# Kernel tuning notes

Measured on AMD Instinct MI355X. Metric: run time of the kernel, lower is better.

The kernel has to match this reference:

```python
import jax, jax.numpy as jnp
import numpy as np

N, E, G = 50000, 800000, 256
H, C = 8, 16
F0 = 64
FH = H * C  # 128
L = 6
EPS = 1e-5
SEL = [0, 1, 2, 3, 4, 5, 5, 5]  # <10 layers -> pad with last


def setup_inputs() -> dict:
    key = jax.random.key(0)
    ks = jax.random.split(key, 32)

    def w(k, shape, fan_in):
        return jax.random.normal(k, shape, jnp.float32) / np.float32(np.sqrt(fan_in))

    inp = {
        'x': jax.random.normal(ks[0], (N, F0), jnp.float32),
        'edge_index': jax.random.randint(ks[1], (2, E), 0, N),
        'batch_vec': jnp.sort(jax.random.randint(ks[2], (N,), 0, G)),
        # layer 0 (in=F0)
        'Wq0': w(ks[3], (F0, FH), F0), 'bq0': 0.01 * jax.random.normal(ks[4], (FH,), jnp.float32),
        'Wk0': w(ks[5], (F0, FH), F0), 'bk0': 0.01 * jax.random.normal(ks[6], (FH,), jnp.float32),
        'Wv0': w(ks[7], (F0, FH), F0), 'bv0': 0.01 * jax.random.normal(ks[8], (FH,), jnp.float32),
        'Ws0': w(ks[9], (F0, FH), F0), 'bs0': 0.01 * jax.random.normal(ks[10], (FH,), jnp.float32),
        # layers 1..L-1 (in=FH), stacked
        'Wq': w(ks[11], (L - 1, FH, FH), FH), 'bq': 0.01 * jax.random.normal(ks[12], (L - 1, FH), jnp.float32),
        'Wk': w(ks[13], (L - 1, FH, FH), FH), 'bk': 0.01 * jax.random.normal(ks[14], (L - 1, FH), jnp.float32),
        'Wv': w(ks[15], (L - 1, FH, FH), FH), 'bv': 0.01 * jax.random.normal(ks[16], (L - 1, FH), jnp.float32),
        'Ws': w(ks[17], (L - 1, FH, FH), FH), 'bs': 0.01 * jax.random.normal(ks[18], (L - 1, FH), jnp.float32),
        # BatchNorm affine params per layer
        'gamma': jnp.ones((L, FH), jnp.float32),
        'beta': jnp.zeros((L, FH), jnp.float32),
    }
    return inp


def _transformer_conv(x, src, dst, Wq, bq, Wk, bk, Wv, bv, Ws, bs):
    # q from target nodes, k/v from source nodes (PyG TransformerConv, concat=True)
    q = (x @ Wq + bq).reshape(-1, H, C)
    k = (x @ Wk + bk).reshape(-1, H, C)
    v = (x @ Wv + bv).reshape(-1, H, C)
    s = jnp.einsum('ehc,ehc->eh', q[dst], k[src]) * np.float32(1.0 / np.sqrt(C))  # [E,H]
    m = jax.ops.segment_max(s, dst, num_segments=N)       # segment softmax over in-edges
    e = jnp.exp(s - m[dst])
    denom = jax.ops.segment_sum(e, dst, num_segments=N)
    alpha = e / jnp.maximum(denom[dst], 1e-16)            # [E,H]
    msg = jax.ops.segment_sum(alpha[:, :, None] * v[src], dst, num_segments=N)  # [N,H,C]
    return msg.reshape(-1, FH) + (x @ Ws + bs)            # root/skip connection


def _bn_relu(x, g, b):
    mu = jnp.mean(x, axis=0)
    var = jnp.var(x, axis=0)  # biased, as used for normalization in training mode
    return jax.nn.relu((x - mu) * jax.lax.rsqrt(var + EPS) * g + b)


def reference(x, edge_index, batch_vec, Wq0, bq0, Wk0, bk0, Wv0, bv0, Ws0, bs0,
              Wq, bq, Wk, bk, Wv, bv, Ws, bs, gamma, beta):
    src, dst = edge_index[0], edge_index[1]
    outs = []
    h = _bn_relu(_transformer_conv(x, src, dst, Wq0, bq0, Wk0, bk0, Wv0, bv0, Ws0, bs0),
                 gamma[0], beta[0])
    outs.append(h)
    for i in range(L - 1):
        h = _bn_relu(_transformer_conv(h, src, dst, Wq[i], bq[i], Wk[i], bk[i],
                                       Wv[i], bv[i], Ws[i], bs[i]),
                     gamma[i + 1], beta[i + 1])
        outs.append(h)
    counts = jnp.maximum(jax.ops.segment_sum(jnp.ones((N,), x.dtype), batch_vec, num_segments=G), 1.0)
    pooled = [jax.ops.segment_sum(o, batch_vec, num_segments=G) / counts[:, None] for o in outs]
    latent = jnp.stack([pooled[i] for i in SEL], axis=1)  # [G, 8, FH]
    return latent.reshape(G, -1)                          # [G, 8*FH]
```

## Files before the change

### kernel.cpp

```cpp
#include <hip/hip_runtime.h>
#include <hip/hip_bf16.h>
#include <math.h>

#define NN 50000
#define NE 800000
#define NG 256
#define FHH 128
#define NL 6
#define NCH 49
#define NB 391

typedef __attribute__((ext_vector_type(8))) short s16x8;
typedef __attribute__((ext_vector_type(4))) float f32x4;

#define QSCALE 0.36067376022224085f

#if defined(__has_builtin)
#if __has_builtin(__builtin_amdgcn_fdot2_f32_bf16)
#define HAVE_BFDOT 1
#endif
#endif
#ifndef HAVE_BFDOT
#define HAVE_BFDOT 0
#endif

__device__ __forceinline__ ushort f2bf(float x) {
  uint u = __float_as_uint(x);
  u += 0x7fffu + ((u >> 16) & 1u);
  return (ushort)(u >> 16);
}
__device__ __forceinline__ float bf2f(ushort h) {
  return __uint_as_float(((uint)h) << 16);
}
__device__ __forceinline__ float bfl(uint u) { return __uint_as_float(u << 16); }
__device__ __forceinline__ float bfh(uint u) { return __uint_as_float(u & 0xffff0000u); }
__device__ __forceinline__ uint packbf(float a, float b) {
  return (uint)f2bf(a) | ((uint)f2bf(b) << 16);
}

#if HAVE_BFDOT
typedef __attribute__((ext_vector_type(2))) __bf16 bf16v2;
__device__ __forceinline__ float dot2acc(uint a, uint b, float acc) {
  return __builtin_amdgcn_fdot2_f32_bf16(__builtin_bit_cast(bf16v2, a),
                                         __builtin_bit_cast(bf16v2, b), acc, false);
}
#endif

__device__ __forceinline__ void gload16(const ushort* g, ushort* l) {
  __builtin_amdgcn_global_load_lds(
      (const __attribute__((address_space(1))) uint*)(const void*)g,
      (__attribute__((address_space(3))) uint*)(void*)l, 16, 0, 0);
}

__global__ void k_gstart(const int* __restrict__ bv, int* __restrict__ gstart) {
  int g = blockIdx.x * blockDim.x + threadIdx.x;
  if (g > NG) return;
  int lo = 0, hi = NN;
  while (lo < hi) { int mid = (lo + hi) >> 1; if (bv[mid] < g) lo = mid + 1; else hi = mid; }
  gstart[g] = lo;
}

__global__ void k_deg(const int* __restrict__ dstv, int* __restrict__ deg) {
  int e = blockIdx.x * blockDim.x + threadIdx.x;
  if (e < NE) atomicAdd(&deg[dstv[e]], 1);
}

__global__ __launch_bounds__(256) void k_scanA(const int* __restrict__ deg, int* __restrict__ part) {
  int b = blockIdx.x, t = threadIdx.x;
  int s = 0;
  for (int j = t; j < 1024; j += 256) { int i = b * 1024 + j; if (i < NN) s += deg[i]; }
  __shared__ int sh[4];
  for (int o = 32; o; o >>= 1) s += __shfl_down(s, o, 64);
  if ((t & 63) == 0) sh[t >> 6] = s;
  __syncthreads();
  if (t == 0) part[b] = sh[0] + sh[1] + sh[2] + sh[3];
}

__global__ void k_scanB(int* __restrict__ part, int* __restrict__ row_ptr) {
  if (threadIdx.x == 0 && blockIdx.x == 0) {
    int run = 0;
    for (int i = 0; i < NCH; ++i) { int v = part[i]; part[i] = run; run += v; }
    row_ptr[NN] = run;
  }
}

__global__ __launch_bounds__(1024) void k_scanC(const int* __restrict__ deg, const int* __restrict__ part,
                                                int* __restrict__ row_ptr, int* __restrict__ cursor) {
  __shared__ int buf[1024];
  int b = blockIdx.x, t = threadIdx.x;
  int i = b * 1024 + t;
  int v = (i < NN) ? deg[i] : 0;
  buf[t] = v;
  __syncthreads();
  for (int off = 1; off < 1024; off <<= 1) {
    int add = (t >= off) ? buf[t - off] : 0;
    __syncthreads();
    buf[t] += add;
    __syncthreads();
  }
  if (i < NN) { int ex = part[b] + buf[t] - v; row_ptr[i] = ex; cursor[i] = ex; }
}

__global__ void k_scatter(const int* __restrict__ srcv, const int* __restrict__ dstv,
                          int* __restrict__ cursor, uint* __restrict__ colb) {
  int e = blockIdx.x * blockDim.x + threadIdx.x;
  if (e < NE) {
    int d = dstv[e];
    int pos = atomicAdd(&cursor[d], 1);
    colb[pos] = ((uint)srcv[e]) << 9;
  }
}

__device__ __forceinline__ size_t wtile_idx(int k, int c) {
  return (size_t)(k >> 5) * 4096 + ((((c >> 4) * 4 + ((k & 31) >> 3)) * 16 + (c & 15)) * 8 + (k & 7));
}

__global__ __launch_bounds__(256) void k_wconv0(const float* __restrict__ W0, const float* __restrict__ W1,
                                                const float* __restrict__ W2, const float* __restrict__ W3,
                                                ushort* __restrict__ wh, ushort* __restrict__ wl) {
  int id = blockIdx.x * 256 + threadIdx.x;
  if (id >= 4 * 64 * 128) return;
  int mat = id >> 13, rem = id & 8191;
  int k = rem >> 7, c = rem & 127;
  const float* W = (mat == 0) ? W0 : (mat == 1) ? W1 : (mat == 2) ? W2 : W3;
  float v = W[k * 128 + c];
  ushort h = f2bf(v);
  ushort lo = f2bf(v - bf2f(h));
  size_t dst = (size_t)mat * 8192 + wtile_idx(k, c);
  wh[dst] = h; wl[dst] = lo;
}

__global__ __launch_bounds__(256) void k_wconvS(const float* __restrict__ Wq, const float* __restrict__ Wk,
                                                const float* __restrict__ Wv, const float* __restrict__ Ws,
                                                ushort* __restrict__ wh, ushort* __restrict__ wl) {
  int id = blockIdx.x * 256 + threadIdx.x;
  if (id >= 5 * 4 * 16384) return;
  int lay = id / 65536, rem = id % 65536;
  int mat = rem >> 14, rem2 = rem & 16383;
  int k = rem2 >> 7, c = rem2 & 127;
  const float* W = (mat == 0) ? Wq : (mat == 1) ? Wk : (mat == 2) ? Wv : Ws;
  float v = W[(size_t)lay * 16384 + k * 128 + c];
  ushort h = f2bf(v);
  ushort lo = f2bf(v - bf2f(h));
  size_t dst = 32768 + ((size_t)lay * 4 + mat) * 16384 + wtile_idx(k, c);
  wh[dst] = h; wl[dst] = lo;
}

template <int K>
__global__ __launch_bounds__(256) void k_presplit(const float* __restrict__ Y,
                                                  ushort* __restrict__ Xh) {
  const int CP = K / 4;
  int idx = blockIdx.x * 256 + threadIdx.x;
  int row = idx / CP;
  int c4 = (idx % CP) * 4;
  if (row >= NN) return;
  float4 v = *reinterpret_cast<const float4*>(Y + (size_t)row * K + c4);
  ushort h0 = f2bf(v.x), h1 = f2bf(v.y), h2 = f2bf(v.z), h3 = f2bf(v.w);
  int b = row >> 7, g = (row & 127) >> 4, frow = row & 15;
  int ks = c4 >> 5, qq = (c4 & 31) >> 3, j = c4 & 7;
  size_t base = ((size_t)ks * NB + b) * 4096 + (((g * 4 + qq) * 16) + frow) * 8 + j;
  *reinterpret_cast<uint2*>(Xh + base) =
      make_uint2((uint)h0 | ((uint)h1 << 16), (uint)h2 | ((uint)h3 << 16));
}

template <int K>
__global__ __launch_bounds__(256, 3) void k_gemm(
    const ushort* __restrict__ Xh,
    const ushort* __restrict__ Wth, const ushort* __restrict__ Wtl,
    const float* __restrict__ b0, const float* __restrict__ b1,
    const float* __restrict__ b2, const float* __restrict__ b3,
    ushort* __restrict__ qbf, ushort* __restrict__ kv, ushort* __restrict__ xsb) {
  __shared__ __align__(16) ushort Ah[4096];
  __shared__ __align__(16) ushort Bh[4096];
  __shared__ __align__(16) ushort Bl[4096];
  int bid = blockIdx.x;
  int mat = (bid >> 3) & 3;
  int b = (bid & 7) + ((bid >> 5) << 3);
  if (b >= NB) return;
  int t = threadIdx.x;
  int lane = t & 63, w = t >> 6;
  int wr = w >> 1, wc = w & 1;
  int frow = lane & 15;
  const ushort* wh = Wth + (size_t)mat * (K * 128);
  const ushort* wl = Wtl + (size_t)mat * (K * 128);
  const float* bb = (mat == 0) ? b0 : (mat == 1) ? b1 : (mat == 2) ? b2 : b3;

  f32x4 acc[4][4];
#pragma unroll
  for (int i = 0; i < 4; ++i)
#pragma unroll
    for (int j = 0; j < 4; ++j)
#pragma unroll
      for (int r = 0; r < 4; ++r) acc[i][j][r] = 0.f;

  int wofs = w * 1024 + lane * 8;
  for (int ks = 0; ks < K / 32; ++ks) {
    size_t abase = ((size_t)ks * NB + b) * 4096;
    const ushort* gAh = Xh + abase + wofs;
    const ushort* gBh = wh + ks * 4096 + wofs;
    const ushort* gBl = wl + ks * 4096 + wofs;
    gload16(gAh, &Ah[w * 1024]);
    gload16(gAh + 512, &Ah[w * 1024 + 512]);
    gload16(gBh, &Bh[w * 1024]);
    gload16(gBh + 512, &Bh[w * 1024 + 512]);
    gload16(gBl, &Bl[w * 1024]);
    gload16(gBl + 512, &Bl[w * 1024 + 512]);
    __syncthreads();
    s16x8 ah[4], bh[4], bl[4];
#pragma unroll
    for (int g = 0; g < 4; ++g) {
      ah[g] = *reinterpret_cast<const s16x8*>(&Ah[(wr * 4 + g) * 512 + lane * 8]);
      bh[g] = *reinterpret_cast<const s16x8*>(&Bh[(wc * 4 + g) * 512 + lane * 8]);
      bl[g] = *reinterpret_cast<const s16x8*>(&Bl[(wc * 4 + g) * 512 + lane * 8]);
    }
#pragma unroll
    for (int rg = 0; rg < 4; ++rg)
#pragma unroll
      for (int cg = 0; cg < 4; ++cg) {
        acc[rg][cg] = __builtin_amdgcn_mfma_f32_16x16x32_bf16(ah[rg], bh[cg], acc[rg][cg], 0, 0, 0);
        acc[rg][cg] = __builtin_amdgcn_mfma_f32_16x16x32_bf16(ah[rg], bl[cg], acc[rg][cg], 0, 0, 0);
      }
    __syncthreads();
  }
  int r0 = b * 128;
  int qq = (lane >> 4) << 2;
#pragma unroll
  for (int rg = 0; rg < 4; ++rg) {
#pragma unroll
    for (int cg = 0; cg < 4; ++cg) {
      int colg = wc * 64 + cg * 16 + frow;
      float bv = bb[colg];
#pragma unroll
      for (int r = 0; r < 4; ++r) {
        int row = r0 + wr * 64 + rg * 16 + qq + r;
        if (row >= NN) continue;
        float val = acc[rg][cg][r] + bv;
        if (mat == 0)      qbf[(size_t)row * FHH + colg] = f2bf(val * QSCALE);
        else if (mat == 3) xsb[(size_t)row * FHH + colg] = f2bf(val);
        else {
          int pos = (colg >> 1) * 4 + ((mat == 2) ? 2 : 0) + (colg & 1);
          kv[(size_t)row * 256 + pos] = f2bf(val);
        }
      }
    }
  }
}

__global__ __launch_bounds__(256) void k_agg(const uint* __restrict__ qb,
                                             const ushort* __restrict__ kv,
                                             const uint* __restrict__ xsb,
                                             const int* __restrict__ row_ptr,
                                             const uint* __restrict__ colb,
                                             uint* __restrict__ yb) {
  int n = blockIdx.x * 4 + (threadIdx.x >> 6);
  int lane = threadIdx.x & 63;
  int hl = lane & 31, half = lane >> 5;
  uint2 qp = *reinterpret_cast<const uint2*>(qb + (n << 6) + 2 * hl);
#if !HAVE_BFDOT
  float qa = bfl(qp.x), qbv = bfh(qp.x), qc = bfl(qp.y), qd = bfh(qp.y);
#endif
  const char* kvb = (const char*)kv;
  uint tof = (uint)hl * 16u;
  int e0 = row_ptr[n], e1 = row_ptr[n + 1];
  float sum = 0.f, a0 = 0.f, a1 = 0.f, a2 = 0.f, a3 = 0.f;
  int i = e0;
#define QKDOT(d, p)                                                    \
  {                                                                    \
    p = qa * bfl(d.x);                                                 \
    p = fmaf(qbv, bfh(d.x), p);                                        \
    p = fmaf(qc, bfl(d.z), p);                                         \
    p = fmaf(qd, bfh(d.z), p);                                         \
  }
  for (; i + 8 <= e1; i += 8) {
    uint oA = colb[i + half] + tof;
    uint oB = colb[i + 2 + half] + tof;
    uint oC = colb[i + 4 + half] + tof;
    uint oD = colb[i + 6 + half] + tof;
    uint4 dA = *(const uint4*)(kvb + oA);
    uint4 dB = *(const uint4*)(kvb + oB);
    uint4 dC = *(const uint4*)(kvb + oC);
    uint4 dD = *(const uint4*)(kvb + oD);
    float pA, pB, pC, pD;
#if HAVE_BFDOT
    pA = dot2acc(dA.z, qp.y, dot2acc(dA.x, qp.x, 0.f));
    pB = dot2acc(dB.z, qp.y, dot2acc(dB.x, qp.x, 0.f));
    pC = dot2acc(dC.z, qp.y, dot2acc(dC.x, qp.x, 0.f));
    pD = dot2acc(dD.z, qp.y, dot2acc(dD.x, qp.x, 0.f));
#else
    QKDOT(dA, pA) QKDOT(dB, pB) QKDOT(dC, pC) QKDOT(dD, pD)
#endif
    pA += __shfl_xor(pA, 1, 4);  pB += __shfl_xor(pB, 1, 4);
    pC += __shfl_xor(pC, 1, 4);  pD += __shfl_xor(pD, 1, 4);
    pA += __shfl_xor(pA, 2, 4);  pB += __shfl_xor(pB, 2, 4);
    pC += __shfl_xor(pC, 2, 4);  pD += __shfl_xor(pD, 2, 4);
    float wA = exp2f(fminf(pA, 110.f));
    float wB = exp2f(fminf(pB, 110.f));
    float wC = exp2f(fminf(pC, 110.f));
    float wD = exp2f(fminf(pD, 110.f));
    sum += (wA + wB) + (wC + wD);
    a0 = fmaf(wA, bfl(dA.y), fmaf(wB, bfl(dB.y), fmaf(wC, bfl(dC.y), fmaf(wD, bfl(dD.y), a0))));
    a1 = fmaf(wA, bfh(dA.y), fmaf(wB, bfh(dB.y), fmaf(wC, bfh(dC.y), fmaf(wD, bfh(dD.y), a1))));
    a2 = fmaf(wA, bfl(dA.w), fmaf(wB, bfl(dB.w), fmaf(wC, bfl(dC.w), fmaf(wD, bfl(dD.w), a2))));
    a3 = fmaf(wA, bfh(dA.w), fmaf(wB, bfh(dB.w), fmaf(wC, bfh(dC.w), fmaf(wD, bfh(dD.w), a3))));
  }
  for (; i + 2 <= e1; i += 2) {
    uint oA = colb[i + half] + tof;
    uint4 dA = *(const uint4*)(kvb + oA);
    float pA;
#if HAVE_BFDOT
    pA = dot2acc(dA.z, qp.y, dot2acc(dA.x, qp.x, 0.f));
#else
    QKDOT(dA, pA)
#endif
    pA += __shfl_xor(pA, 1, 4);
    pA += __shfl_xor(pA, 2, 4);
    float wA = exp2f(fminf(pA, 110.f));
    sum += wA;
    a0 = fmaf(wA, bfl(dA.y), a0);
    a1 = fmaf(wA, bfh(dA.y), a1);
    a2 = fmaf(wA, bfl(dA.w), a2);
    a3 = fmaf(wA, bfh(dA.w), a3);
  }
  if (i < e1) {
    uint oA = colb[i] + tof;
    uint4 dA = *(const uint4*)(kvb + oA);
    float pA;
#if HAVE_BFDOT
    pA = dot2acc(dA.z, qp.y, dot2acc(dA.x, qp.x, 0.f));
#else
    QKDOT(dA, pA)
#endif
    pA += __shfl_xor(pA, 1, 4);
    pA += __shfl_xor(pA, 2, 4);
    float wA = exp2f(fminf(pA, 110.f));
    if (half) wA = 0.f;
    sum += wA;
    a0 = fmaf(wA, bfl(dA.y), a0);
    a1 = fmaf(wA, bfh(dA.y), a1);
    a2 = fmaf(wA, bfl(dA.w), a2);
    a3 = fmaf(wA, bfh(dA.w), a3);
  }
#undef QKDOT
  sum += __shfl_xor(sum, 32);
  a0 += __shfl_xor(a0, 32);
  a1 += __shfl_xor(a1, 32);
  a2 += __shfl_xor(a2, 32);
  a3 += __shfl_xor(a3, 32);
  float inv = 1.f / fmaxf(sum, 1e-16f);
  uint2 xv = *reinterpret_cast<const uint2*>(xsb + (n << 6) + 2 * hl);
  float o0 = fmaf(a0, inv, bfl(xv.x));
  float o1 = fmaf(a1, inv, bfh(xv.x));
  float o2 = fmaf(a2, inv, bfl(xv.y));
  float o3 = fmaf(a3, inv, bfh(xv.y));
  if (half == 0) {
    uint2 o;
    o.x = packbf(o0, o1);
    o.y = packbf(o2, o3);
    *reinterpret_cast<uint2*>(yb + (n << 6) + 2 * hl) = o;
  }
}

__global__ __launch_bounds__(256) void k_bnstats(const uint* __restrict__ yb,
                                                 float* __restrict__ stats) {
  __shared__ float2 s1[256], s2[256];
  int u = threadIdx.x & 63;
  int grp = threadIdx.x >> 6;
  float2 a = make_float2(0.f, 0.f), b = make_float2(0.f, 0.f);
  for (int r = blockIdx.x * 4 + grp; r < NN; r += 1024) {
    uint d = yb[(size_t)r * 64 + u];
    float x = bfl(d), yv = bfh(d);
    a.x += x; a.y += yv;
    b.x = fmaf(x, x, b.x); b.y = fmaf(yv, yv, b.y);
  }
  s1[threadIdx.x] = a;
  s2[threadIdx.x] = b;
  __syncthreads();
  if (grp == 0) {
#pragma unroll
    for (int g = 1; g < 4; ++g) {
      a.x += s1[u + 64 * g].x; a.y += s1[u + 64 * g].y;
      b.x += s2[u + 64 * g].x; b.y += s2[u + 64 * g].y;
    }
    atomicAdd(&stats[2 * u], a.x);
    atomicAdd(&stats[2 * u + 1], a.y);
    atomicAdd(&stats[128 + 2 * u], b.x);
    atomicAdd(&stats[128 + 2 * u + 1], b.y);
  }
}

template <int WRITE_X>
__global__ __launch_bounds__(256) void k_post(const uint* __restrict__ yb,
                                              const float* __restrict__ st,
                                              const float* __restrict__ gvec,
                                              const float* __restrict__ bvec_,
                                              const int* __restrict__ bv,
                                              const int* __restrict__ gstart,
                                              float* __restrict__ out, int layer,
                                              ushort* __restrict__ Xh) {
  __shared__ float acts[8][128];
  __shared__ int sg[8];
  __shared__ float ssc[128], ssh[128];
  int b = blockIdx.x, t = threadIdx.x;
  if (t < 128) {
    const float invn = 1.f / (float)NN;
    float mu = st[t] * invn;
    float var = st[128 + t] * invn - mu * mu;
    float sc = gvec[t] * rsqrtf(var + 1e-5f);
    ssc[t] = sc;
    ssh[t] = bvec_[t] - mu * sc;
  }
  if (t < 8) sg[t] = (b * 8 + t < NN) ? bv[b * 8 + t] : -1;
  __syncthreads();
  int row = b * 8 + (t >> 5);
  int c4 = (t & 31) * 4;
  bool ok = row < NN;
  float4 a = make_float4(0.f, 0.f, 0.f, 0.f);
  if (ok) {
    uint2 u2 = *reinterpret_cast<const uint2*>(yb + (size_t)row * 64 + (c4 >> 1));
    a.x = fmaxf(fmaf(bfl(u2.x), ssc[c4 + 0], ssh[c4 + 0]), 0.f);
    a.y = fmaxf(fmaf(bfh(u2.x), ssc[c4 + 1], ssh[c4 + 1]), 0.f);
    a.z = fmaxf(fmaf(bfl(u2.y), ssc[c4 + 2], ssh[c4 + 2]), 0.f);
    a.w = fmaxf(fmaf(bfh(u2.y), ssc[c4 + 3], ssh[c4 + 3]), 0.f);
  }
  *reinterpret_cast<float4*>(&acts[t >> 5][c4]) = a;
  if (WRITE_X && ok) {
    ushort h0 = f2bf(a.x), h1 = f2bf(a.y), h2 = f2bf(a.z), h3 = f2bf(a.w);
    int bb = row >> 7, g = (row & 127) >> 4, frow = row & 15;
    int ks = c4 >> 5, qq = (c4 & 31) >> 3, j = c4 & 7;
    size_t base = ((size_t)ks * NB + bb) * 4096 + (((g * 4 + qq) * 16) + frow) * 8 + j;
    *reinterpret_cast<uint2*>(Xh + base) =
        make_uint2((uint)h0 | ((uint)h1 << 16), (uint)h2 | ((uint)h3 << 16));
  }
  __syncthreads();
  if (t < 128) {
    float racc = 0.f;
    int cg = sg[0];
    for (int r = 0; r < 8; ++r) {
      int g = sg[r];
      if (g != cg) {
        if (cg >= 0) {
          float p = racc / (float)(gstart[cg + 1] - gstart[cg]);
          if (layer < 5) atomicAdd(&out[(size_t)cg * 1024 + layer * FHH + t], p);
          else {
            atomicAdd(&out[(size_t)cg * 1024 + 5 * FHH + t], p);
            atomicAdd(&out[(size_t)cg * 1024 + 6 * FHH + t], p);
            atomicAdd(&out[(size_t)cg * 1024 + 7 * FHH + t], p);
          }
        }
        racc = 0.f;
        cg = g;
      }
      racc += acts[r][t];
    }
    if (cg >= 0) {
      float p = racc / (float)(gstart[cg + 1] - gstart[cg]);
      if (layer < 5) atomicAdd(&out[(size_t)cg * 1024 + layer * FHH + t], p);
      else {
        atomicAdd(&out[(size_t)cg * 1024 + 5 * FHH + t], p);
        atomicAdd(&out[(size_t)cg * 1024 + 6 * FHH + t], p);
        atomicAdd(&out[(size_t)cg * 1024 + 7 * FHH + t], p);
      }
    }
  }
}

extern "C" void kernel_launch(void* const* d_in, const int* in_sizes, int n_in,
                              void* d_out, int out_size, void* d_ws, size_t ws_size,
                              hipStream_t stream) {
  (void)in_sizes; (void)n_in; (void)ws_size;
  const float* x    = (const float*)d_in[0];
  const int*   ei   = (const int*)d_in[1];
  const int*   bvec = (const int*)d_in[2];
  const float* Wq0  = (const float*)d_in[3];
  const float* bq0  = (const float*)d_in[4];
  const float* Wk0  = (const float*)d_in[5];
  const float* bk0  = (const float*)d_in[6];
  const float* Wv0  = (const float*)d_in[7];
  const float* bv0  = (const float*)d_in[8];
  const float* Ws0  = (const float*)d_in[9];
  const float* bs0  = (const float*)d_in[10];
  const float* WqS  = (const float*)d_in[11];
  const float* bqS  = (const float*)d_in[12];
  const float* WkS  = (const float*)d_in[13];
  const float* bkS  = (const float*)d_in[14];
  const float* WvS  = (const float*)d_in[15];
  const float* bvS  = (const float*)d_in[16];
  const float* WsS  = (const float*)d_in[17];
  const float* bsS  = (const float*)d_in[18];
  const float* gamma = (const float*)d_in[19];
  const float* beta  = (const float*)d_in[20];
  float* out = (float*)d_out;

  char* ws = (char*)d_ws;
  size_t off = 0;
  auto alloc = [&](size_t bytes) {
    void* p = ws + off;
    off = (off + bytes + 255) & ~(size_t)255;
    return p;
  };
  ushort* qbf = (ushort*)alloc((size_t)NN * FHH * 2);
  ushort* xsb = (ushort*)alloc((size_t)NN * FHH * 2);
  uint* yb    = (uint*)alloc((size_t)NN * 64 * 4);
  ushort* kv  = (ushort*)alloc((size_t)NN * 256 * 2);
  ushort* Xh  = (ushort*)alloc((size_t)4 * NB * 4096 * 2 + 8192);
  uint* colb   = (uint*)alloc((size_t)NE * 4);
  int* row_ptr = (int*)alloc((size_t)(NN + 1) * 4);
  int* cursor  = (int*)alloc((size_t)NN * 4);
  int* deg     = (int*)alloc((size_t)NN * 4);
  int* part    = (int*)alloc((size_t)NCH * 4);
  int* gstart  = (int*)alloc((size_t)(NG + 1) * 4);
  float* bstat = (float*)alloc((size_t)NL * 2 * FHH * 4);
  ushort* wsh = (ushort*)alloc((size_t)360448 * 2);
  ushort* wsl = (ushort*)alloc((size_t)360448 * 2);

  const int* srcv = ei;
  const int* dstv = ei + NE;

  hipMemsetAsync(out, 0, (size_t)out_size * 4, stream);
  hipMemsetAsync(deg, 0, (size_t)NN * 4, stream);
  hipMemsetAsync(bstat, 0, (size_t)NL * 2 * FHH * 4, stream);
  k_gstart<<<5, 64, 0, stream>>>(bvec, gstart);
  k_deg<<<(NE + 255) / 256, 256, 0, stream>>>(dstv, deg);
  k_scanA<<<NCH, 256, 0, stream>>>(deg, part);
  k_scanB<<<1, 64, 0, stream>>>(part, row_ptr);
  k_scanC<<<NCH, 1024, 0, stream>>>(deg, part, row_ptr, cursor);
  k_scatter<<<(NE + 255) / 256, 256, 0, stream>>>(srcv, dstv, cursor, colb);
  k_wconv0<<<128, 256, 0, stream>>>(Wq0, Wk0, Wv0, Ws0, wsh, wsl);
  k_wconvS<<<1280, 256, 0, stream>>>(WqS, WkS, WvS, WsS, wsh, wsl);
  k_presplit<64><<<(NN * 16 + 255) / 256, 256, 0, stream>>>(x, Xh);

  const int GEMM_GRID = 49 * 32;
  for (int l = 0; l < NL; ++l) {
    const ushort* WthL = wsh + ((l == 0) ? 0 : (size_t)32768 + (size_t)(l - 1) * 65536);
    const ushort* WtlL = wsl + ((l == 0) ? 0 : (size_t)32768 + (size_t)(l - 1) * 65536);
    const float *bq_, *bk_, *bv_, *bs_;
    if (l == 0) { bq_ = bq0; bk_ = bk0; bv_ = bv0; bs_ = bs0; }
    else {
      size_t bo = (size_t)(l - 1) * FHH;
      bq_ = bqS + bo; bk_ = bkS + bo; bv_ = bvS + bo; bs_ = bsS + bo;
    }
    if (l == 0)
      k_gemm<64><<<GEMM_GRID, 256, 0, stream>>>(Xh, WthL, WtlL, bq_, bk_, bv_, bs_, qbf, kv, xsb);
    else
      k_gemm<128><<<GEMM_GRID, 256, 0, stream>>>(Xh, WthL, WtlL, bq_, bk_, bv_, bs_, qbf, kv, xsb);
    k_agg<<<NN / 4, 256, 0, stream>>>((const uint*)qbf, kv, (const uint*)xsb, row_ptr, colb, yb);
    float* lstat = bstat + (size_t)l * 2 * FHH;
    k_bnstats<<<256, 256, 0, stream>>>(yb, lstat);
    if (l + 1 < NL)
      k_post<1><<<6250, 256, 0, stream>>>(yb, lstat, gamma + (size_t)l * FHH,
                                          beta + (size_t)l * FHH, bvec, gstart, out, l, Xh);
    else
      k_post<0><<<6250, 256, 0, stream>>>(yb, lstat, gamma + (size_t)l * FHH,
                                          beta + (size_t)l * FHH, bvec, gstart, out, l, Xh);
  }
}
```

Measured before the change: 901.3 us.

## Remap edge aggregation lanes to four edges per wavefront with wider loads

Restructures the per-node attention aggregation kernel so each wavefront processes four edges at once, with 16 lanes per edge and each lane holding 8 features, instead of two edges with 32 lanes of 4 features. This cuts the cross-lane reduction for the per-head dot product from two shuffle steps to one and makes the gathered K/V loads 32 bytes per lane. It also drops the bf16 dot2 builtin path in favour of plain FMAs and adds a second shuffle stage to combine the four edge groups at the end. In exchange it doubles accumulator registers and leaves more lanes idle on the tail for nodes with few in-edges.

```diff
diff --git a/kernel.cpp b/kernel.cpp
--- a/kernel.cpp
+++ b/kernel.cpp
@@ -15,15 +15,6 @@
 
 #define QSCALE 0.36067376022224085f
 
-#if defined(__has_builtin)
-#if __has_builtin(__builtin_amdgcn_fdot2_f32_bf16)
-#define HAVE_BFDOT 1
-#endif
-#endif
-#ifndef HAVE_BFDOT
-#define HAVE_BFDOT 0
-#endif
-
 __device__ __forceinline__ ushort f2bf(float x) {
   uint u = __float_as_uint(x);
   u += 0x7fffu + ((u >> 16) & 1u);
@@ -37,14 +28,6 @@
 __device__ __forceinline__ uint packbf(float a, float b) {
   return (uint)f2bf(a) | ((uint)f2bf(b) << 16);
 }
-
-#if HAVE_BFDOT
-typedef __attribute__((ext_vector_type(2))) __bf16 bf16v2;
-__device__ __forceinline__ float dot2acc(uint a, uint b, float acc) {
-  return __builtin_amdgcn_fdot2_f32_bf16(__builtin_bit_cast(bf16v2, a),
-                                         __builtin_bit_cast(bf16v2, b), acc, false);
-}
-#endif
 
 __device__ __forceinline__ void gload16(const ushort* g, ushort* l) {
   __builtin_amdgcn_global_load_lds(
@@ -254,109 +237,103 @@
                                              uint* __restrict__ yb) {
   int n = blockIdx.x * 4 + (threadIdx.x >> 6);
   int lane = threadIdx.x & 63;
-  int hl = lane & 31, half = lane >> 5;
-  uint2 qp = *reinterpret_cast<const uint2*>(qb + (n << 6) + 2 * hl);
-#if !HAVE_BFDOT
-  float qa = bfl(qp.x), qbv = bfh(qp.x), qc = bfl(qp.y), qd = bfh(qp.y);
-#endif
+  int q_ = lane >> 4, ql = lane & 15;
+  uint4 qp = *reinterpret_cast<const uint4*>(qb + (n << 6) + 4 * ql);
+  float q0 = bfl(qp.x), q1 = bfh(qp.x), q2 = bfl(qp.y), q3 = bfh(qp.y);
+  float q4 = bfl(qp.z), q5 = bfh(qp.z), q6 = bfl(qp.w), q7 = bfh(qp.w);
   const char* kvb = (const char*)kv;
-  uint tof = (uint)hl * 16u;
+  uint tof = (uint)ql * 32u;
   int e0 = row_ptr[n], e1 = row_ptr[n + 1];
-  float sum = 0.f, a0 = 0.f, a1 = 0.f, a2 = 0.f, a3 = 0.f;
+  float sum = 0.f;
+  float a0 = 0.f, a1 = 0.f, a2 = 0.f, a3 = 0.f;
+  float a4 = 0.f, a5 = 0.f, a6 = 0.f, a7 = 0.f;
   int i = e0;
-#define QKDOT(d, p)                                                    \
-  {                                                                    \
-    p = qa * bfl(d.x);                                                 \
-    p = fmaf(qbv, bfh(d.x), p);                                        \
-    p = fmaf(qc, bfl(d.z), p);                                         \
-    p = fmaf(qd, bfh(d.z), p);                                         \
+#define EDOT(d0, d1, p)                         \
+  {                                             \
+    p = q0 * bfl(d0.x);                         \
+    p = fmaf(q1, bfh(d0.x), p);                 \
+    p = fmaf(q2, bfl(d0.z), p);                 \
+    p = fmaf(q3, bfh(d0.z), p);                 \
+    p = fmaf(q4, bfl(d1.x), p);                 \
+    p = fmaf(q5, bfh(d1.x), p);                 \
+    p = fmaf(q6, bfl(d1.z), p);                 \
+    p = fmaf(q7, bfh(d1.z), p);                 \
+  }
+#define EACC(d0, d1, wv)                        \
+  {                                             \
+    a0 = fmaf(wv, bfl(d0.y), a0);               \
+    a1 = fmaf(wv, bfh(d0.y), a1);               \
+    a2 = fmaf(wv, bfl(d0.w), a2);               \
+    a3 = fmaf(wv, bfh(d0.w), a3);               \
+    a4 = fmaf(wv, bfl(d1.y), a4);               \
+    a5 = fmaf(wv, bfh(d1.y), a5);               \
+    a6 = fmaf(wv, bfl(d1.w), a6);               \
+    a7 = fmaf(wv, bfh(d1.w), a7);               \
   }
   for (; i + 8 <= e1; i += 8) {
-    uint oA = colb[i + half] + tof;
-    uint oB = colb[i + 2 + half] + tof;
-    uint oC = colb[i + 4 + half] + tof;
-    uint oD = colb[i + 6 + half] + tof;
-    uint4 dA = *(const uint4*)(kvb + oA);
-    uint4 dB = *(const uint4*)(kvb + oB);
-    uint4 dC = *(const uint4*)(kvb + oC);
-    uint4 dD = *(const uint4*)(kvb + oD);
-    float pA, pB, pC, pD;
-#if HAVE_BFDOT
-    pA = dot2acc(dA.z, qp.y, dot2acc(dA.x, qp.x, 0.f));
-    pB = dot2acc(dB.z, qp.y, dot2acc(dB.x, qp.x, 0.f));
-    pC = dot2acc(dC.z, qp.y, dot2acc(dC.x, qp.x, 0.f));
-    pD = dot2acc(dD.z, qp.y, dot2acc(dD.x, qp.x, 0.f));
-#else
-    QKDOT(dA, pA) QKDOT(dB, pB) QKDOT(dC, pC) QKDOT(dD, pD)
-#endif
-    pA += __shfl_xor(pA, 1, 4);  pB += __shfl_xor(pB, 1, 4);
-    pC += __shfl_xor(pC, 1, 4);  pD += __shfl_xor(pD, 1, 4);
-    pA += __shfl_xor(pA, 2, 4);  pB += __shfl_xor(pB, 2, 4);
-    pC += __shfl_xor(pC, 2, 4);  pD += __shfl_xor(pD, 2, 4);
+    uint oA = colb[i + q_] + tof;
+    uint oB = colb[i + 4 + q_] + tof;
+    uint4 dA0 = *(const uint4*)(kvb + oA);
+    uint4 dA1 = *(const uint4*)(kvb + oA + 16);
+    uint4 dB0 = *(const uint4*)(kvb + oB);
+    uint4 dB1 = *(const uint4*)(kvb + oB + 16);
+    float pA, pB;
+    EDOT(dA0, dA1, pA)
+    EDOT(dB0, dB1, pB)
+    pA += __shfl_xor(pA, 1, 2);
+    pB += __shfl_xor(pB, 1, 2);
     float wA = exp2f(fminf(pA, 110.f));
     float wB = exp2f(fminf(pB, 110.f));
-    float wC = exp2f(fminf(pC, 110.f));
-    float wD = exp2f(fminf(pD, 110.f));
-    sum += (wA + wB) + (wC + wD);
-    a0 = fmaf(wA, bfl(dA.y), fmaf(wB, bfl(dB.y), fmaf(wC, bfl(dC.y), fmaf(wD, bfl(dD.y), a0))));
-    a1 = fmaf(wA, bfh(dA.y), fmaf(wB, bfh(dB.y), fmaf(wC, bfh(dC.y), fmaf(wD, bfh(dD.y), a1))));
-    a2 = fmaf(wA, bfl(dA.w), fmaf(wB, bfl(dB.w), fmaf(wC, bfl(dC.w), fmaf(wD, bfl(dD.w), a2))));
-    a3 = fmaf(wA, bfh(dA.w), fmaf(wB, bfh(dB.w), fmaf(wC, bfh(dC.w), fmaf(wD, bfh(dD.w), a3))));
-  }
-  for (; i + 2 <= e1; i += 2) {
-    uint oA = colb[i + half] + tof;
-    uint4 dA = *(const uint4*)(kvb + oA);
+    sum += wA + wB;
+    EACC(dA0, dA1, wA)
+    EACC(dB0, dB1, wB)
+  }
+  if (i + 4 <= e1) {
+    uint oA = colb[i + q_] + tof;
+    uint4 dA0 = *(const uint4*)(kvb + oA);
+    uint4 dA1 = *(const uint4*)(kvb + oA + 16);
     float pA;
-#if HAVE_BFDOT
-    pA = dot2acc(dA.z, qp.y, dot2acc(dA.x, qp.x, 0.f));
-#else
-    QKDOT(dA, pA)
-#endif
-    pA += __shfl_xor(pA, 1, 4);
-    pA += __shfl_xor(pA, 2, 4);
+    EDOT(dA0, dA1, pA)
+    pA += __shfl_xor(pA, 1, 2);
     float wA = exp2f(fminf(pA, 110.f));
     sum += wA;
-    a0 = fmaf(wA, bfl(dA.y), a0);
-    a1 = fmaf(wA, bfh(dA.y), a1);
-    a2 = fmaf(wA, bfl(dA.w), a2);
-    a3 = fmaf(wA, bfh(dA.w), a3);
+    EACC(dA0, dA1, wA)
+    i += 4;
   }
   if (i < e1) {
-    uint oA = colb[i] + tof;
-    uint4 dA = *(const uint4*)(kvb + oA);
+    int idx = i + q_;
+    bool valid = idx < e1;
+    uint oA = colb[valid ? idx : e0] + tof;
+    uint4 dA0 = *(const uint4*)(kvb + oA);
+    uint4 dA1 = *(const uint4*)(kvb + oA + 16);
     float pA;
-#if HAVE_BFDOT
-    pA = dot2acc(dA.z, qp.y, dot2acc(dA.x, qp.x, 0.f));
-#else
-    QKDOT(dA, pA)
-#endif
-    pA += __shfl_xor(pA, 1, 4);
-    pA += __shfl_xor(pA, 2, 4);
+    EDOT(dA0, dA1, pA)
+    pA += __shfl_xor(pA, 1, 2);
     float wA = exp2f(fminf(pA, 110.f));
-    if (half) wA = 0.f;
+    if (!valid) wA = 0.f;
     sum += wA;
-    a0 = fmaf(wA, bfl(dA.y), a0);
-    a1 = fmaf(wA, bfh(dA.y), a1);
-    a2 = fmaf(wA, bfl(dA.w), a2);
-    a3 = fmaf(wA, bfh(dA.w), a3);
-  }
-#undef QKDOT
-  sum += __shfl_xor(sum, 32);
-  a0 += __shfl_xor(a0, 32);
-  a1 += __shfl_xor(a1, 32);
-  a2 += __shfl_xor(a2, 32);
-  a3 += __shfl_xor(a3, 32);
-  float inv = 1.f / fmaxf(sum, 1e-16f);
-  uint2 xv = *reinterpret_cast<const uint2*>(xsb + (n << 6) + 2 * hl);
-  float o0 = fmaf(a0, inv, bfl(xv.x));
-  float o1 = fmaf(a1, inv, bfh(xv.x));
-  float o2 = fmaf(a2, inv, bfl(xv.y));
-  float o3 = fmaf(a3, inv, bfh(xv.y));
-  if (half == 0) {
-    uint2 o;
-    o.x = packbf(o0, o1);
-    o.y = packbf(o2, o3);
-    *reinterpret_cast<uint2*>(yb + (n << 6) + 2 * hl) = o;
+    EACC(dA0, dA1, wA)
+  }
+#undef EDOT
+#undef EACC
+  sum += __shfl_xor(sum, 16);  sum += __shfl_xor(sum, 32);
+  a0 += __shfl_xor(a0, 16);    a0 += __shfl_xor(a0, 32);
+  a1 += __shfl_xor(a1, 16);    a1 += __shfl_xor(a1, 32);
+  a2 += __shfl_xor(a2, 16);    a2 += __shfl_xor(a2, 32);
+  a3 += __shfl_xor(a3, 16);    a3 += __shfl_xor(a3, 32);
+  a4 += __shfl_xor(a4, 16);    a4 += __shfl_xor(a4, 32);
+  a5 += __shfl_xor(a5, 16);    a5 += __shfl_xor(a5, 32);
+  a6 += __shfl_xor(a6, 16);    a6 += __shfl_xor(a6, 32);
+  a7 += __shfl_xor(a7, 16);    a7 += __shfl_xor(a7, 32);
+  if (q_ == 0) {
+    float inv = 1.f / fmaxf(sum, 1e-16f);
+    uint4 xv = *reinterpret_cast<const uint4*>(xsb + (n << 6) + 4 * ql);
+    uint4 o;
+    o.x = packbf(fmaf(a0, inv, bfl(xv.x)), fmaf(a1, inv, bfh(xv.x)));
+    o.y = packbf(fmaf(a2, inv, bfl(xv.y)), fmaf(a3, inv, bfh(xv.y)));
+    o.z = packbf(fmaf(a4, inv, bfl(xv.z)), fmaf(a5, inv, bfh(xv.z)));
+    o.w = packbf(fmaf(a6, inv, bfl(xv.w)), fmaf(a7, inv, bfh(xv.w)));
+    *reinterpret_cast<uint4*>(yb + (n << 6) + 4 * ql) = o;
   }
 }
 
```

After: 910.3 us. No clear change (+1.0%).

## Fuse BatchNorm statistics into aggregation kernel with persistent grid

Applied to the files above, without the earlier changes.

The aggregation kernel now runs as a persistent grid of 2048 blocks looping over node groups and accumulates per-channel sum and sum-of-squares of its fp32 outputs. It reduces them in shared memory and atomically adds them into 8 striped stat copies, which the post kernel sums. This removes the separate k_bnstats launch and its re-read of yb each layer. It also drops the bf16 dot2 intrinsic path in favour of scalar FMAs, and stats now come from unrounded fp32 values instead of the bf16-stored ones.

```diff
diff --git a/kernel.cpp b/kernel.cpp
--- a/kernel.cpp
+++ b/kernel.cpp
@@ -9,20 +9,12 @@
 #define NL 6
 #define NCH 49
 #define NB 391
+#define NAGG 2048
 
 typedef __attribute__((ext_vector_type(8))) short s16x8;
 typedef __attribute__((ext_vector_type(4))) float f32x4;
 
 #define QSCALE 0.36067376022224085f
-
-#if defined(__has_builtin)
-#if __has_builtin(__builtin_amdgcn_fdot2_f32_bf16)
-#define HAVE_BFDOT 1
-#endif
-#endif
-#ifndef HAVE_BFDOT
-#define HAVE_BFDOT 0
-#endif
 
 __device__ __forceinline__ ushort f2bf(float x) {
   uint u = __float_as_uint(x);
@@ -37,14 +29,6 @@
 __device__ __forceinline__ uint packbf(float a, float b) {
   return (uint)f2bf(a) | ((uint)f2bf(b) << 16);
 }
-
-#if HAVE_BFDOT
-typedef __attribute__((ext_vector_type(2))) __bf16 bf16v2;
-__device__ __forceinline__ float dot2acc(uint a, uint b, float acc) {
-  return __builtin_amdgcn_fdot2_f32_bf16(__builtin_bit_cast(bf16v2, a),
-                                         __builtin_bit_cast(bf16v2, b), acc, false);
-}
-#endif
 
 __device__ __forceinline__ void gload16(const ushort* g, ushort* l) {
   __builtin_amdgcn_global_load_lds(
@@ -251,140 +235,126 @@
                                              const uint* __restrict__ xsb,
                                              const int* __restrict__ row_ptr,
                                              const uint* __restrict__ colb,
-                                             uint* __restrict__ yb) {
-  int n = blockIdx.x * 4 + (threadIdx.x >> 6);
-  int lane = threadIdx.x & 63;
+                                             uint* __restrict__ yb,
+                                             float* __restrict__ stats) {
+  __shared__ float sred[4][32][8];
+  int t = threadIdx.x;
+  int wv = t >> 6;
+  int lane = t & 63;
   int hl = lane & 31, half = lane >> 5;
-  uint2 qp = *reinterpret_cast<const uint2*>(qb + (n << 6) + 2 * hl);
-#if !HAVE_BFDOT
-  float qa = bfl(qp.x), qbv = bfh(qp.x), qc = bfl(qp.y), qd = bfh(qp.y);
-#endif
+  uint tof = (uint)hl * 16u;
   const char* kvb = (const char*)kv;
-  uint tof = (uint)hl * 16u;
-  int e0 = row_ptr[n], e1 = row_ptr[n + 1];
-  float sum = 0.f, a0 = 0.f, a1 = 0.f, a2 = 0.f, a3 = 0.f;
-  int i = e0;
-#define QKDOT(d, p)                                                    \
-  {                                                                    \
-    p = qa * bfl(d.x);                                                 \
-    p = fmaf(qbv, bfh(d.x), p);                                        \
-    p = fmaf(qc, bfl(d.z), p);                                         \
-    p = fmaf(qd, bfh(d.z), p);                                         \
-  }
-  for (; i + 8 <= e1; i += 8) {
-    uint oA = colb[i + half] + tof;
-    uint oB = colb[i + 2 + half] + tof;
-    uint oC = colb[i + 4 + half] + tof;
-    uint oD = colb[i + 6 + half] + tof;
-    uint4 dA = *(const uint4*)(kvb + oA);
-    uint4 dB = *(const uint4*)(kvb + oB);
-    uint4 dC = *(const uint4*)(kvb + oC);
-    uint4 dD = *(const uint4*)(kvb + oD);
-    float pA, pB, pC, pD;
-#if HAVE_BFDOT
-    pA = dot2acc(dA.z, qp.y, dot2acc(dA.x, qp.x, 0.f));
-    pB = dot2acc(dB.z, qp.y, dot2acc(dB.x, qp.x, 0.f));
-    pC = dot2acc(dC.z, qp.y, dot2acc(dC.x, qp.x, 0.f));
-    pD = dot2acc(dD.z, qp.y, dot2acc(dD.x, qp.x, 0.f));
-#else
-    QKDOT(dA, pA) QKDOT(dB, pB) QKDOT(dC, pC) QKDOT(dD, pD)
-#endif
-    pA += __shfl_xor(pA, 1, 4);  pB += __shfl_xor(pB, 1, 4);
-    pC += __shfl_xor(pC, 1, 4);  pD += __shfl_xor(pD, 1, 4);
-    pA += __shfl_xor(pA, 2, 4);  pB += __shfl_xor(pB, 2, 4);
-    pC += __shfl_xor(pC, 2, 4);  pD += __shfl_xor(pD, 2, 4);
-    float wA = exp2f(fminf(pA, 110.f));
-    float wB = exp2f(fminf(pB, 110.f));
-    float wC = exp2f(fminf(pC, 110.f));
-    float wD = exp2f(fminf(pD, 110.f));
-    sum += (wA + wB) + (wC + wD);
-    a0 = fmaf(wA, bfl(dA.y), fmaf(wB, bfl(dB.y), fmaf(wC, bfl(dC.y), fmaf(wD, bfl(dD.y), a0))));
-    a1 = fmaf(wA, bfh(dA.y), fmaf(wB, bfh(dB.y), fmaf(wC, bfh(dC.y), fmaf(wD, bfh(dD.y), a1))));
-    a2 = fmaf(wA, bfl(dA.w), fmaf(wB, bfl(dB.w), fmaf(wC, bfl(dC.w), fmaf(wD, bfl(dD.w), a2))));
-    a3 = fmaf(wA, bfh(dA.w), fmaf(wB, bfh(dB.w), fmaf(wC, bfh(dC.w), fmaf(wD, bfh(dD.w), a3))));
-  }
-  for (; i + 2 <= e1; i += 2) {
-    uint oA = colb[i + half] + tof;
-    uint4 dA = *(const uint4*)(kvb + oA);
-    float pA;
-#if HAVE_BFDOT
-    pA = dot2acc(dA.z, qp.y, dot2acc(dA.x, qp.x, 0.f));
-#else
-    QKDOT(dA, pA)
-#endif
-    pA += __shfl_xor(pA, 1, 4);
-    pA += __shfl_xor(pA, 2, 4);
-    float wA = exp2f(fminf(pA, 110.f));
-    sum += wA;
-    a0 = fmaf(wA, bfl(dA.y), a0);
-    a1 = fmaf(wA, bfh(dA.y), a1);
-    a2 = fmaf(wA, bfl(dA.w), a2);
-    a3 = fmaf(wA, bfh(dA.w), a3);
-  }
-  if (i < e1) {
-    uint oA = colb[i] + tof;
-    uint4 dA = *(const uint4*)(kvb + oA);
-    float pA;
-#if HAVE_BFDOT
-    pA = dot2acc(dA.z, qp.y, dot2acc(dA.x, qp.x, 0.f));
-#else
-    QKDOT(dA, pA)
-#endif
-    pA += __shfl_xor(pA, 1, 4);
-    pA += __shfl_xor(pA, 2, 4);
-    float wA = exp2f(fminf(pA, 110.f));
-    if (half) wA = 0.f;
-    sum += wA;
-    a0 = fmaf(wA, bfl(dA.y), a0);
-    a1 = fmaf(wA, bfh(dA.y), a1);
-    a2 = fmaf(wA, bfl(dA.w), a2);
-    a3 = fmaf(wA, bfh(dA.w), a3);
-  }
+  float s0 = 0.f, s1 = 0.f, s2 = 0.f, s3 = 0.f;
+  float ss0 = 0.f, ss1 = 0.f, ss2 = 0.f, ss3 = 0.f;
+
+  for (int ng = blockIdx.x; ng < NN / 4; ng += NAGG) {
+    int n = ng * 4 + wv;
+    uint2 qp = *reinterpret_cast<const uint2*>(qb + (n << 6) + 2 * hl);
+    float qa = bfl(qp.x), qbv = bfh(qp.x), qc = bfl(qp.y), qd = bfh(qp.y);
+    int e0 = row_ptr[n], e1 = row_ptr[n + 1];
+    float sum = 0.f, a0 = 0.f, a1 = 0.f, a2 = 0.f, a3 = 0.f;
+    int i = e0;
+#define QKDOT(d, p)                                                  \
+    {                                                                \
+      p = qa * bfl(d.x);                                             \
+      p = fmaf(qbv, bfh(d.x), p);                                    \
+      p = fmaf(qc, bfl(d.z), p);                                     \
+      p = fmaf(qd, bfh(d.z), p);                                     \
+    }
+    for (; i + 8 <= e1; i += 8) {
+      uint oA = colb[i + half] + tof;
+      uint oB = colb[i + 2 + half] + tof;
+      uint oC = colb[i + 4 + half] + tof;
+      uint oD = colb[i + 6 + half] + tof;
+      uint4 dA = *(const uint4*)(kvb + oA);
+      uint4 dB = *(const uint4*)(kvb + oB);
+      uint4 dC = *(const uint4*)(kvb + oC);
+      uint4 dD = *(const uint4*)(kvb + oD);
+      float pA, pB, pC, pD;
+      QKDOT(dA, pA) QKDOT(dB, pB) QKDOT(dC, pC) QKDOT(dD, pD)
+      pA += __shfl_xor(pA, 1, 4);  pB += __shfl_xor(pB, 1, 4);
+      pC += __shfl_xor(pC, 1, 4);  pD += __shfl_xor(pD, 1, 4);
+      pA += __shfl_xor(pA, 2, 4);  pB += __shfl_xor(pB, 2, 4);
+      pC += __shfl_xor(pC, 2, 4);  pD += __shfl_xor(pD, 2, 4);
+      float wA = exp2f(fminf(pA, 110.f));
+      float wB = exp2f(fminf(pB, 110.f));
+      float wC = exp2f(fminf(pC, 110.f));
+      float wD = exp2f(fminf(pD, 110.f));
+      sum += (wA + wB) + (wC + wD);
+      a0 = fmaf(wA, bfl(dA.y), fmaf(wB, bfl(dB.y), fmaf(wC, bfl(dC.y), fmaf(wD, bfl(dD.y), a0))));
+      a1 = fmaf(wA, bfh(dA.y), fmaf(wB, bfh(dB.y), fmaf(wC, bfh(dC.y), fmaf(wD, bfh(dD.y), a1))));
+      a2 = fmaf(wA, bfl(dA.w), fmaf(wB, bfl(dB.w), fmaf(wC, bfl(dC.w), fmaf(wD, bfl(dD.w), a2))));
+      a3 = fmaf(wA, bfh(dA.w), fmaf(wB, bfh(dB.w), fmaf(wC, bfh(dC.w), fmaf(wD, bfh(dD.w), a3))));
+    }
+    for (; i + 2 <= e1; i += 2) {
+      uint oA = colb[i + half] + tof;
+      uint4 dA = *(const uint4*)(kvb + oA);
+      float pA;
+      QKDOT(dA, pA)
+      pA += __shfl_xor(pA, 1, 4);
+      pA += __shfl_xor(pA, 2, 4);
+      float wA = exp2f(fminf(pA, 110.f));
+      sum += wA;
+      a0 = fmaf(wA, bfl(dA.y), a0);
+      a1 = fmaf(wA, bfh(dA.y), a1);
+      a2 = fmaf(wA, bfl(dA.w), a2);
+      a3 = fmaf(wA, bfh(dA.w), a3);
+    }
+    if (i < e1) {
+      uint oA = colb[i] + tof;
+      uint4 dA = *(const uint4*)(kvb + oA);
+      float pA;
+      QKDOT(dA, pA)
+      pA += __shfl_xor(pA, 1, 4);
+      pA += __shfl_xor(pA, 2, 4);
+      float wA = exp2f(fminf(pA, 110.f));
+      if (half) wA = 0.f;
+      sum += wA;
+      a0 = fmaf(wA, bfl(dA.y), a0);
+      a1 = fmaf(wA, bfh(dA.y), a1);
+      a2 = fmaf(wA, bfl(dA.w), a2);
+      a3 = fmaf(wA, bfh(dA.w), a3);
+    }
 #undef QKDOT
-  sum += __shfl_xor(sum, 32);
-  a0 += __shfl_xor(a0, 32);
-  a1 += __shfl_xor(a1, 32);
-  a2 += __shfl_xor(a2, 32);
-  a3 += __shfl_xor(a3, 32);
-  float inv = 1.f / fmaxf(sum, 1e-16f);
-  uint2 xv = *reinterpret_cast<const uint2*>(xsb + (n << 6) + 2 * hl);
-  float o0 = fmaf(a0, inv, bfl(xv.x));
-  float o1 = fmaf(a1, inv, bfh(xv.x));
-  float o2 = fmaf(a2, inv, bfl(xv.y));
-  float o3 = fmaf(a3, inv, bfh(xv.y));
+    sum += __shfl_xor(sum, 32);
+    a0 += __shfl_xor(a0, 32);
+    a1 += __shfl_xor(a1, 32);
+    a2 += __shfl_xor(a2, 32);
+    a3 += __shfl_xor(a3, 32);
+    float inv = 1.f / fmaxf(sum, 1e-16f);
+    uint2 xv = *reinterpret_cast<const uint2*>(xsb + (n << 6) + 2 * hl);
+    float o0 = fmaf(a0, inv, bfl(xv.x));
+    float o1 = fmaf(a1, inv, bfh(xv.x));
+    float o2 = fmaf(a2, inv, bfl(xv.y));
+    float o3 = fmaf(a3, inv, bfh(xv.y));
+    if (half == 0) {
+      uint2 o;
+      o.x = packbf(o0, o1);
+      o.y = packbf(o2, o3);
+      *reinterpret_cast<uint2*>(yb + (n << 6) + 2 * hl) = o;
+      s0 += o0; s1 += o1; s2 += o2; s3 += o3;
+      ss0 = fmaf(o0, o0, ss0);
+      ss1 = fmaf(o1, o1, ss1);
+      ss2 = fmaf(o2, o2, ss2);
+      ss3 = fmaf(o3, o3, ss3);
+    }
+  }
   if (half == 0) {
-    uint2 o;
-    o.x = packbf(o0, o1);
-    o.y = packbf(o2, o3);
-    *reinterpret_cast<uint2*>(yb + (n << 6) + 2 * hl) = o;
-  }
-}
-
-__global__ __launch_bounds__(256) void k_bnstats(const uint* __restrict__ yb,
-                                                 float* __restrict__ stats) {
-  __shared__ float2 s1[256], s2[256];
-  int u = threadIdx.x & 63;
-  int grp = threadIdx.x >> 6;
-  float2 a = make_float2(0.f, 0.f), b = make_float2(0.f, 0.f);
-  for (int r = blockIdx.x * 4 + grp; r < NN; r += 1024) {
-    uint d = yb[(size_t)r * 64 + u];
-    float x = bfl(d), yv = bfh(d);
-    a.x += x; a.y += yv;
-    b.x = fmaf(x, x, b.x); b.y = fmaf(yv, yv, b.y);
-  }
-  s1[threadIdx.x] = a;
-  s2[threadIdx.x] = b;
+    sred[wv][hl][0] = s0;  sred[wv][hl][1] = s1;
+    sred[wv][hl][2] = s2;  sred[wv][hl][3] = s3;
+    sred[wv][hl][4] = ss0; sred[wv][hl][5] = ss1;
+    sred[wv][hl][6] = ss2; sred[wv][hl][7] = ss3;
+  }
   __syncthreads();
-  if (grp == 0) {
-#pragma unroll
-    for (int g = 1; g < 4; ++g) {
-      a.x += s1[u + 64 * g].x; a.y += s1[u + 64 * g].y;
-      b.x += s2[u + 64 * g].x; b.y += s2[u + 64 * g].y;
-    }
-    atomicAdd(&stats[2 * u], a.x);
-    atomicAdd(&stats[2 * u + 1], a.y);
-    atomicAdd(&stats[128 + 2 * u], b.x);
-    atomicAdd(&stats[128 + 2 * u + 1], b.y);
+  if (t < 32) {
+    float* st = stats + (blockIdx.x & 7) * 256;
+#pragma unroll
+    for (int j = 0; j < 4; ++j) {
+      float vs = sred[0][t][j] + sred[1][t][j] + sred[2][t][j] + sred[3][t][j];
+      float vq = sred[0][t][4 + j] + sred[1][t][4 + j] + sred[2][t][4 + j] + sred[3][t][4 + j];
+      atomicAdd(&st[4 * t + j], vs);
+      atomicAdd(&st[128 + 4 * t + j], vq);
+    }
   }
 }
 
@@ -402,9 +372,12 @@
   __shared__ float ssc[128], ssh[128];
   int b = blockIdx.x, t = threadIdx.x;
   if (t < 128) {
+    float s = 0.f, q = 0.f;
+#pragma unroll
+    for (int c = 0; c < 8; ++c) { s += st[c * 256 + t]; q += st[c * 256 + 128 + t]; }
     const float invn = 1.f / (float)NN;
-    float mu = st[t] * invn;
-    float var = st[128 + t] * invn - mu * mu;
+    float mu = s * invn;
+    float var = q * invn - mu * mu;
     float sc = gvec[t] * rsqrtf(var + 1e-5f);
     ssc[t] = sc;
     ssh[t] = bvec_[t] - mu * sc;
@@ -509,7 +482,7 @@
   int* deg     = (int*)alloc((size_t)NN * 4);
   int* part    = (int*)alloc((size_t)NCH * 4);
   int* gstart  = (int*)alloc((size_t)(NG + 1) * 4);
-  float* bstat = (float*)alloc((size_t)NL * 2 * FHH * 4);
+  float* bstat = (float*)alloc((size_t)NL * 8 * 256 * 4);
   ushort* wsh = (ushort*)alloc((size_t)360448 * 2);
   ushort* wsl = (ushort*)alloc((size_t)360448 * 2);
 
@@ -518,7 +491,7 @@
 
   hipMemsetAsync(out, 0, (size_t)out_size * 4, stream);
   hipMemsetAsync(deg, 0, (size_t)NN * 4, stream);
-  hipMemsetAsync(bstat, 0, (size_t)NL * 2 * FHH * 4, stream);
+  hipMemsetAsync(bstat, 0, (size_t)NL * 8 * 256 * 4, stream);
   k_gstart<<<5, 64, 0, stream>>>(bvec, gstart);
   k_deg<<<(NE + 255) / 256, 256, 0, stream>>>(dstv, deg);
   k_scanA<<<NCH, 256, 0, stream>>>(deg, part);
@@ -543,9 +516,8 @@
       k_gemm<64><<<GEMM_GRID, 256, 0, stream>>>(Xh, WthL, WtlL, bq_, bk_, bv_, bs_, qbf, kv, xsb);
     else
       k_gemm<128><<<GEMM_GRID, 256, 0, stream>>>(Xh, WthL, WtlL, bq_, bk_, bv_, bs_, qbf, kv, xsb);
-    k_agg<<<NN / 4, 256, 0, stream>>>((const uint*)qbf, kv, (const uint*)xsb, row_ptr, colb, yb);
-    float* lstat = bstat + (size_t)l * 2 * FHH;
-    k_bnstats<<<256, 256, 0, stream>>>(yb, lstat);
+    float* lstat = bstat + (size_t)l * 8 * 256;
+    k_agg<<<NAGG, 256, 0, stream>>>((const uint*)qbf, kv, (const uint*)xsb, row_ptr, colb, yb, lstat);
     if (l + 1 < NL)
       k_post<1><<<6250, 256, 0, stream>>>(yb, lstat, gamma + (size_t)l * FHH,
                                           beta + (size_t)l * FHH, bvec, gstart, out, l, Xh);
```

Measured after the change: 933.4 us. +3.6%, slower.
